# Performance work log

Hardware: AMD Instinct MI355X
Metric: run time of the kernel (lower is better)

The kernel has to match this reference:

```python
import jax, jax.numpy as jnp
import numpy as np

N, D = 12288, 128
T = 0.07  # temperature from __init__ default


def setup_inputs() -> dict:
    key = jax.random.key(0)
    x = jax.random.normal(key, (N, D), dtype=jnp.float32)
    # L2-normalize rows (this loss is defined on unit-norm embeddings;
    # keeps exp(sim / 0.07) finite in fp32 while preserving the exact math).
    x = x / jnp.linalg.norm(x, axis=-1, keepdims=True)
    return {"x": x}


def reference(x):
    # x: [N, D] -> sim: [N, N]
    sim = jnp.matmul(x, x.T) / T
    # faithful to torch: exp -> sum over last dim -> log -> mean (no LSE stabilization)
    return jnp.mean(jnp.log(jnp.sum(jnp.exp(sim), axis=-1)))
```

## Files before the change

### kernel.cpp

```cpp
#include <hip/hip_runtime.h>
#include <hip/hip_bf16.h>

#define NROWS 12288
#define DDIM  128
#define NT    96
#define CHUNK 4
#define NBLK  1200

typedef __bf16 bf16x8 __attribute__((ext_vector_type(8)));
typedef float  f32x4  __attribute__((ext_vector_type(4)));

#define GLD_LDS(g, l) __builtin_amdgcn_global_load_lds(                      \
    (const __attribute__((address_space(1))) void*)(g),                      \
    (__attribute__((address_space(3))) void*)(l), 16, 0, 0)

__device__ __forceinline__ unsigned short f2bf(float f) {
    union { float f; unsigned u; } a; a.f = f;
    unsigned r = a.u + 0x7fffu + ((a.u >> 16) & 1u);
    return (unsigned short)(r >> 16);
}

__global__ void convert_kernel(const float* __restrict__ x, unsigned short* __restrict__ xb,
                               float* __restrict__ rowsum, float* __restrict__ out) {
    int gid = blockIdx.x * 256 + threadIdx.x;
    int i = gid * 4;
    float4 v = *(const float4*)(x + i);
    ushort4 o;
    o.x = f2bf(v.x); o.y = f2bf(v.y); o.z = f2bf(v.z); o.w = f2bf(v.w);
    *(ushort4*)(xb + i) = o;
    if (gid < NROWS) rowsum[gid] = 0.f;
    if (gid == 0) out[0] = 0.f;
}

__device__ __forceinline__ void stage_tile(const unsigned short* __restrict__ xb,
                                           int row0, unsigned short* lds,
                                           int wave, int lane) {
    #pragma unroll
    for (int it = 0; it < 8; ++it) {
        int rbase = wave * 32 + it * 4;
        int r = rbase + (lane >> 4);
        int chunk = (lane & 15) ^ (r & 7);
        GLD_LDS(xb + (size_t)(row0 + r) * DDIM + chunk * 8, lds + rbase * DDIM);
    }
}

__global__ __launch_bounds__(256, 2) void gemm_exp_rowsum(
    const unsigned short* __restrict__ xb, float* __restrict__ rowsum)
{
    __shared__ __align__(16) unsigned short As[128 * DDIM];
    __shared__ __align__(16) unsigned short Bs[128 * DDIM];
    __shared__ float csumS[CHUNK * 128];
    __shared__ float rsum[128];

    const int tid = threadIdx.x;

    int rem = blockIdx.x, bi = 0;
    for (;;) {
        int nch = (NT - bi + CHUNK - 1) / CHUNK;
        if (rem < nch) break;
        rem -= nch; ++bi;
    }
    const int jt0 = bi + rem * CHUNK;
    const int ntiles = min(CHUNK, NT - jt0);
    const int i0 = bi * 128;

    for (int k = tid; k < CHUNK * 128; k += 256) csumS[k] = 0.f;
    if (tid < 128) rsum[tid] = 0.f;

    const int wave = tid >> 6, lane = tid & 63;
    const int wm = wave >> 1, wn = wave & 1;
    const int m16 = lane & 15, q = lane >> 4;

    stage_tile(xb, i0, As, wave, lane);
    stage_tile(xb, jt0 * 128, Bs, wave, lane);
    __syncthreads();

    bf16x8 af[4][4];
    #pragma unroll
    for (int mi = 0; mi < 4; ++mi) {
        int r = wm * 64 + mi * 16 + m16;
        #pragma unroll
        for (int ks = 0; ks < 4; ++ks)
            af[mi][ks] = *(const bf16x8*)(&As[r * DDIM + (((ks * 4 + q) ^ (r & 7)) * 8)]);
    }
    __syncthreads();

    const float SCALE = 20.609929155556625f;

    f32x4 rp4[4];
    #pragma unroll
    for (int mi = 0; mi < 4; ++mi) rp4[mi] = (f32x4){0.f, 0.f, 0.f, 0.f};

    unsigned short* curB = Bs;
    unsigned short* nxtB = As;

    for (int t = 0; t < ntiles; ++t) {
        const int jt = jt0 + t;

        if (t + 1 < ntiles) stage_tile(xb, (jt + 1) * 128, nxtB, wave, lane);

        f32x4 acc[4][4] = {};
        #pragma unroll
        for (int ks = 0; ks < 4; ++ks) {
            bf16x8 bfr[4];
            #pragma unroll
            for (int ni = 0; ni < 4; ++ni) {
                int r = wn * 64 + ni * 16 + m16;
                bfr[ni] = *(const bf16x8*)(&curB[r * DDIM + (((ks * 4 + q) ^ (r & 7)) * 8)]);
            }
            __builtin_amdgcn_s_setprio(1);
            #pragma unroll
            for (int mi = 0; mi < 4; ++mi)
                #pragma unroll
                for (int ni = 0; ni < 4; ++ni)
                    acc[mi][ni] = __builtin_amdgcn_mfma_f32_16x16x32_bf16(
                        af[mi][ks], bfr[ni], acc[mi][ni], 0, 0, 0);
            __builtin_amdgcn_s_setprio(0);
        }

        f32x4 cp4[4];
        #pragma unroll
        for (int ni = 0; ni < 4; ++ni) cp4[ni] = (f32x4){0.f, 0.f, 0.f, 0.f};

        #pragma unroll
        for (int mi = 0; mi < 4; ++mi)
            #pragma unroll
            for (int ni = 0; ni < 4; ++ni) {
                f32x4 sv = acc[mi][ni] * SCALE;
                f32x4 ev;
                ev[0] = __builtin_amdgcn_exp2f(sv[0]);
                ev[1] = __builtin_amdgcn_exp2f(sv[1]);
                ev[2] = __builtin_amdgcn_exp2f(sv[2]);
                ev[3] = __builtin_amdgcn_exp2f(sv[3]);
                rp4[mi] += ev;
                cp4[ni] += ev;
            }

        if (jt != bi) {
            #pragma unroll
            for (int ni = 0; ni < 4; ++ni) {
                float s = (cp4[ni][0] + cp4[ni][1]) + (cp4[ni][2] + cp4[ni][3]);
                s += __shfl_xor(s, 16);
                s += __shfl_xor(s, 32);
                if (q == 0) atomicAdd(&csumS[t * 128 + wn * 64 + ni * 16 + m16], s);
            }
        }

        __syncthreads();
        unsigned short* tmp = curB; curB = nxtB; nxtB = tmp;
    }

    #pragma unroll
    for (int mi = 0; mi < 4; ++mi)
        #pragma unroll
        for (int r = 0; r < 4; ++r) {
            float s = rp4[mi][r];
            s += __shfl_xor(s, 1);
            s += __shfl_xor(s, 2);
            s += __shfl_xor(s, 4);
            s += __shfl_xor(s, 8);
            if (m16 == 0) atomicAdd(&rsum[wm * 64 + mi * 16 + q * 4 + r], s);
        }
    __syncthreads();

    if (tid < 128) atomicAdd(&rowsum[i0 + tid], rsum[tid]);
    for (int k = tid; k < ntiles * 128; k += 256) {
        float v = csumS[k];
        if (v != 0.f) atomicAdd(&rowsum[jt0 * 128 + k], v);
    }
}

__global__ void finalize_kernel(const float* __restrict__ rowsum, float* __restrict__ out) {
    __shared__ float red[4];
    int gid = blockIdx.x * 256 + threadIdx.x;
    float lg = __logf(rowsum[gid]);
    #pragma unroll
    for (int off = 1; off < 64; off <<= 1)
        lg += __shfl_xor(lg, off);
    const int wv = threadIdx.x >> 6, ln = threadIdx.x & 63;
    if (ln == 0) red[wv] = lg;
    __syncthreads();
    if (threadIdx.x == 0)
        atomicAdd(out, (red[0] + red[1] + red[2] + red[3]) * (1.0f / (float)NROWS));
}

extern "C" void kernel_launch(void* const* d_in, const int* in_sizes, int n_in,
                              void* d_out, int out_size, void* d_ws, size_t ws_size,
                              hipStream_t stream) {
    const float* x = (const float*)d_in[0];
    float* out = (float*)d_out;

    float* rowsum = (float*)d_ws;
    unsigned short* xb = (unsigned short*)((char*)d_ws + NROWS * sizeof(float));

    convert_kernel<<<dim3((NROWS * DDIM) / (4 * 256)), dim3(256), 0, stream>>>(x, xb, rowsum, out);
    gemm_exp_rowsum<<<dim3(NBLK), dim3(256), 0, stream>>>(xb, rowsum);
    finalize_kernel<<<dim3(NROWS / 256), dim3(256), 0, stream>>>(rowsum, out);
}
```

Baseline: 105.9 us.

## Halve LDS footprint with 64-row B half-tiles and raise occupancy to four blocks

The symmetric GEMM-exp-rowsum kernel now uses a single 32 KB LDS buffer. The A tile is loaded once into registers, with each wave owning 32 rows, and the buffer is then reused as a double buffer of 64-row B half-tiles. Launch bounds go from 2 to 4 blocks per CU, and each block covers 6 column tiles instead of 4, so 816 blocks are launched instead of 1200. Row sums are atomically added straight to global memory, dropping the LDS rsum stage. The aim is more latency hiding through occupancy and fewer redundant A loads, at the cost of smaller per-wave MFMA tiles and more barriers per tile.

```diff
diff --git a/kernel.cpp b/kernel.cpp
--- a/kernel.cpp
+++ b/kernel.cpp
@@ -4,8 +4,8 @@
 #define NROWS 12288
 #define DDIM  128
 #define NT    96
-#define CHUNK 4
-#define NBLK  1200
+#define CHUNK 6
+#define NBLK  816
 
 typedef __bf16 bf16x8 __attribute__((ext_vector_type(8)));
 typedef float  f32x4  __attribute__((ext_vector_type(4)));
@@ -32,25 +32,11 @@
     if (gid == 0) out[0] = 0.f;
 }
 
-__device__ __forceinline__ void stage_tile(const unsigned short* __restrict__ xb,
-                                           int row0, unsigned short* lds,
-                                           int wave, int lane) {
-    #pragma unroll
-    for (int it = 0; it < 8; ++it) {
-        int rbase = wave * 32 + it * 4;
-        int r = rbase + (lane >> 4);
-        int chunk = (lane & 15) ^ (r & 7);
-        GLD_LDS(xb + (size_t)(row0 + r) * DDIM + chunk * 8, lds + rbase * DDIM);
-    }
-}
-
-__global__ __launch_bounds__(256, 2) void gemm_exp_rowsum(
+__global__ __launch_bounds__(256, 4) void gemm_exp_rowsum(
     const unsigned short* __restrict__ xb, float* __restrict__ rowsum)
 {
-    __shared__ __align__(16) unsigned short As[128 * DDIM];
-    __shared__ __align__(16) unsigned short Bs[128 * DDIM];
+    __shared__ __align__(16) unsigned short smem[128 * DDIM];
     __shared__ float csumS[CHUNK * 128];
-    __shared__ float rsum[128];
 
     const int tid = threadIdx.x;
 
@@ -62,55 +48,74 @@
     }
     const int jt0 = bi + rem * CHUNK;
     const int ntiles = min(CHUNK, NT - jt0);
+    const int H = 2 * ntiles;
     const int i0 = bi * 128;
 
     for (int k = tid; k < CHUNK * 128; k += 256) csumS[k] = 0.f;
-    if (tid < 128) rsum[tid] = 0.f;
 
     const int wave = tid >> 6, lane = tid & 63;
-    const int wm = wave >> 1, wn = wave & 1;
     const int m16 = lane & 15, q = lane >> 4;
 
-    stage_tile(xb, i0, As, wave, lane);
-    stage_tile(xb, jt0 * 128, Bs, wave, lane);
-    __syncthreads();
-
-    bf16x8 af[4][4];
     #pragma unroll
-    for (int mi = 0; mi < 4; ++mi) {
-        int r = wm * 64 + mi * 16 + m16;
-        #pragma unroll
-        for (int ks = 0; ks < 4; ++ks)
-            af[mi][ks] = *(const bf16x8*)(&As[r * DDIM + (((ks * 4 + q) ^ (r & 7)) * 8)]);
+    for (int it = 0; it < 8; ++it) {
+        int rbase = wave * 32 + it * 4;
+        int r = rbase + (lane >> 4);
+        int chunk = (lane & 15) ^ (r & 7);
+        GLD_LDS(xb + (size_t)(i0 + r) * DDIM + chunk * 8, smem + rbase * DDIM);
     }
     __syncthreads();
 
+    bf16x8 af[2][4];
+    #pragma unroll
+    for (int mi = 0; mi < 2; ++mi) {
+        int r = wave * 32 + mi * 16 + m16;
+        #pragma unroll
+        for (int ks = 0; ks < 4; ++ks)
+            af[mi][ks] = *(const bf16x8*)(&smem[r * DDIM + (((ks * 4 + q) ^ (r & 7)) * 8)]);
+    }
+    __syncthreads();
+
+    unsigned short* const buf0 = smem;
+    unsigned short* const buf1 = smem + 64 * DDIM;
+
+    #define STAGE_HALF(h, dst) do {                                              \
+        int jrow0_ = jt0 * 128 + (h) * 64;                                       \
+        _Pragma("unroll")                                                        \
+        for (int it = 0; it < 4; ++it) {                                         \
+            int rbase = wave * 16 + it * 4;                                      \
+            int r = rbase + (lane >> 4);                                         \
+            int chunk = (lane & 15) ^ (r & 7);                                   \
+            GLD_LDS(xb + (size_t)(jrow0_ + r) * DDIM + chunk * 8, (dst) + rbase * DDIM); \
+        }                                                                        \
+    } while (0)
+
+    STAGE_HALF(0, buf0);
+
     const float SCALE = 20.609929155556625f;
 
-    f32x4 rp4[4];
-    #pragma unroll
-    for (int mi = 0; mi < 4; ++mi) rp4[mi] = (f32x4){0.f, 0.f, 0.f, 0.f};
+    f32x4 rp4[2];
+    rp4[0] = (f32x4){0.f, 0.f, 0.f, 0.f};
+    rp4[1] = (f32x4){0.f, 0.f, 0.f, 0.f};
 
-    unsigned short* curB = Bs;
-    unsigned short* nxtB = As;
+    for (int h = 0; h < H; ++h) {
+        __syncthreads();
+        unsigned short* nxt = ((h + 1) & 1) ? buf1 : buf0;
+        if (h + 1 < H) STAGE_HALF(h + 1, nxt);
 
-    for (int t = 0; t < ntiles; ++t) {
-        const int jt = jt0 + t;
+        const unsigned short* cb = (h & 1) ? buf1 : buf0;
 
-        if (t + 1 < ntiles) stage_tile(xb, (jt + 1) * 128, nxtB, wave, lane);
-
-        f32x4 acc[4][4] = {};
+        f32x4 acc[2][4] = {};
         #pragma unroll
         for (int ks = 0; ks < 4; ++ks) {
             bf16x8 bfr[4];
             #pragma unroll
             for (int ni = 0; ni < 4; ++ni) {
-                int r = wn * 64 + ni * 16 + m16;
-                bfr[ni] = *(const bf16x8*)(&curB[r * DDIM + (((ks * 4 + q) ^ (r & 7)) * 8)]);
+                int r = ni * 16 + m16;
+                bfr[ni] = *(const bf16x8*)(&cb[r * DDIM + (((ks * 4 + q) ^ (r & 7)) * 8)]);
             }
             __builtin_amdgcn_s_setprio(1);
             #pragma unroll
-            for (int mi = 0; mi < 4; ++mi)
+            for (int mi = 0; mi < 2; ++mi)
                 #pragma unroll
                 for (int ni = 0; ni < 4; ++ni)
                     acc[mi][ni] = __builtin_amdgcn_mfma_f32_16x16x32_bf16(
@@ -118,12 +123,9 @@
             __builtin_amdgcn_s_setprio(0);
         }
 
-        f32x4 cp4[4];
+        float cp[4] = {0.f, 0.f, 0.f, 0.f};
         #pragma unroll
-        for (int ni = 0; ni < 4; ++ni) cp4[ni] = (f32x4){0.f, 0.f, 0.f, 0.f};
-
-        #pragma unroll
-        for (int mi = 0; mi < 4; ++mi)
+        for (int mi = 0; mi < 2; ++mi)
             #pragma unroll
             for (int ni = 0; ni < 4; ++ni) {
                 f32x4 sv = acc[mi][ni] * SCALE;
@@ -133,25 +135,22 @@
                 ev[2] = __builtin_amdgcn_exp2f(sv[2]);
                 ev[3] = __builtin_amdgcn_exp2f(sv[3]);
                 rp4[mi] += ev;
-                cp4[ni] += ev;
+                cp[ni] += (ev[0] + ev[1]) + (ev[2] + ev[3]);
             }
 
-        if (jt != bi) {
+        if (jt0 + (h >> 1) != bi) {
             #pragma unroll
             for (int ni = 0; ni < 4; ++ni) {
-                float s = (cp4[ni][0] + cp4[ni][1]) + (cp4[ni][2] + cp4[ni][3]);
+                float s = cp[ni];
                 s += __shfl_xor(s, 16);
                 s += __shfl_xor(s, 32);
-                if (q == 0) atomicAdd(&csumS[t * 128 + wn * 64 + ni * 16 + m16], s);
+                if (q == 0) atomicAdd(&csumS[h * 64 + ni * 16 + m16], s);
             }
         }
-
-        __syncthreads();
-        unsigned short* tmp = curB; curB = nxtB; nxtB = tmp;
     }
 
     #pragma unroll
-    for (int mi = 0; mi < 4; ++mi)
+    for (int mi = 0; mi < 2; ++mi)
         #pragma unroll
         for (int r = 0; r < 4; ++r) {
             float s = rp4[mi][r];
@@ -159,11 +158,10 @@
             s += __shfl_xor(s, 2);
             s += __shfl_xor(s, 4);
             s += __shfl_xor(s, 8);
-            if (m16 == 0) atomicAdd(&rsum[wm * 64 + mi * 16 + q * 4 + r], s);
+            if (m16 == 0) atomicAdd(&rowsum[i0 + wave * 32 + mi * 16 + q * 4 + r], s);
         }
+
     __syncthreads();
-
-    if (tid < 128) atomicAdd(&rowsum[i0 + tid], rsum[tid]);
     for (int k = tid; k < ntiles * 128; k += 256) {
         float v = csumS[k];
         if (v != 0.f) atomicAdd(&rowsum[jt0 * 128 + k], v);
```

Result: no change. 104.4 us (-1.4%).

## Pre-pack bf16 operands in MFMA fragment order and load directly from global

Applied to the files above, without the earlier changes.

The convert kernel now writes bf16 data in a fragment-major layout matching the MFMA 16x16x32 operand pattern, so each lane can load its bf16x8 fragment with one coalesced 16-byte global load. The GEMM kernel drops LDS staging, double buffering and the per-tile barrier, and instead reads B fragments straight from global/L2 into registers. The chunk size grows from 4 to 12 tiles per block (432 blocks instead of 1200), and row sums are atomically added directly to global memory instead of through a shared buffer. This removes LDS traffic and synchronization, but global load latency is now exposed with no explicit prefetch, register pressure rises, and fewer, longer blocks can balance load less evenly.

```diff
diff --git a/kernel.cpp b/kernel.cpp
--- a/kernel.cpp
+++ b/kernel.cpp
@@ -4,15 +4,11 @@
 #define NROWS 12288
 #define DDIM  128
 #define NT    96
-#define CHUNK 4
-#define NBLK  1200
+#define CHUNK 12
+#define NBLK  432
 
 typedef __bf16 bf16x8 __attribute__((ext_vector_type(8)));
 typedef float  f32x4  __attribute__((ext_vector_type(4)));
-
-#define GLD_LDS(g, l) __builtin_amdgcn_global_load_lds(                      \
-    (const __attribute__((address_space(1))) void*)(g),                      \
-    (__attribute__((address_space(3))) void*)(l), 16, 0, 0)
 
 __device__ __forceinline__ unsigned short f2bf(float f) {
     union { float f; unsigned u; } a; a.f = f;
@@ -20,37 +16,29 @@
     return (unsigned short)(r >> 16);
 }
 
-__global__ void convert_kernel(const float* __restrict__ x, unsigned short* __restrict__ xb,
+__global__ void convert_kernel(const float* __restrict__ x, unsigned short* __restrict__ xbT,
                                float* __restrict__ rowsum, float* __restrict__ out) {
     int gid = blockIdx.x * 256 + threadIdx.x;
-    int i = gid * 4;
-    float4 v = *(const float4*)(x + i);
-    ushort4 o;
-    o.x = f2bf(v.x); o.y = f2bf(v.y); o.z = f2bf(v.z); o.w = f2bf(v.w);
-    *(ushort4*)(xb + i) = o;
+    int e = gid << 3;
+    float4 v0 = *(const float4*)(x + e);
+    float4 v1 = *(const float4*)(x + e + 4);
+    uint4 o;
+    o.x = (unsigned)f2bf(v0.x) | ((unsigned)f2bf(v0.y) << 16);
+    o.y = (unsigned)f2bf(v0.z) | ((unsigned)f2bf(v0.w) << 16);
+    o.z = (unsigned)f2bf(v1.x) | ((unsigned)f2bf(v1.y) << 16);
+    o.w = (unsigned)f2bf(v1.z) | ((unsigned)f2bf(v1.w) << 16);
+    int r = gid >> 4;
+    int c = gid & 15;
+    size_t off = ((size_t)((r >> 4) * 4 + (c >> 2)) * 64 + (c & 3) * 16 + (r & 15)) * 8;
+    *(uint4*)(xbT + off) = o;
     if (gid < NROWS) rowsum[gid] = 0.f;
     if (gid == 0) out[0] = 0.f;
 }
 
-__device__ __forceinline__ void stage_tile(const unsigned short* __restrict__ xb,
-                                           int row0, unsigned short* lds,
-                                           int wave, int lane) {
-    #pragma unroll
-    for (int it = 0; it < 8; ++it) {
-        int rbase = wave * 32 + it * 4;
-        int r = rbase + (lane >> 4);
-        int chunk = (lane & 15) ^ (r & 7);
-        GLD_LDS(xb + (size_t)(row0 + r) * DDIM + chunk * 8, lds + rbase * DDIM);
-    }
-}
-
 __global__ __launch_bounds__(256, 2) void gemm_exp_rowsum(
-    const unsigned short* __restrict__ xb, float* __restrict__ rowsum)
+    const unsigned short* __restrict__ xbT, float* __restrict__ rowsum)
 {
-    __shared__ __align__(16) unsigned short As[128 * DDIM];
-    __shared__ __align__(16) unsigned short Bs[128 * DDIM];
     __shared__ float csumS[CHUNK * 128];
-    __shared__ float rsum[128];
 
     const int tid = threadIdx.x;
 
@@ -65,23 +53,18 @@
     const int i0 = bi * 128;
 
     for (int k = tid; k < CHUNK * 128; k += 256) csumS[k] = 0.f;
-    if (tid < 128) rsum[tid] = 0.f;
 
     const int wave = tid >> 6, lane = tid & 63;
-    const int wm = wave >> 1, wn = wave & 1;
     const int m16 = lane & 15, q = lane >> 4;
-
-    stage_tile(xb, i0, As, wave, lane);
-    stage_tile(xb, jt0 * 128, Bs, wave, lane);
-    __syncthreads();
+    const int wr = wave >> 1, wc = wave & 1;
 
     bf16x8 af[4][4];
     #pragma unroll
     for (int mi = 0; mi < 4; ++mi) {
-        int r = wm * 64 + mi * 16 + m16;
+        int arb = bi * 8 + wr * 4 + mi;
         #pragma unroll
         for (int ks = 0; ks < 4; ++ks)
-            af[mi][ks] = *(const bf16x8*)(&As[r * DDIM + (((ks * 4 + q) ^ (r & 7)) * 8)]);
+            af[mi][ks] = *(const bf16x8*)(xbT + ((size_t)(arb * 4 + ks) * 64 + lane) * 8);
     }
     __syncthreads();
 
@@ -91,32 +74,26 @@
     #pragma unroll
     for (int mi = 0; mi < 4; ++mi) rp4[mi] = (f32x4){0.f, 0.f, 0.f, 0.f};
 
-    unsigned short* curB = Bs;
-    unsigned short* nxtB = As;
-
     for (int t = 0; t < ntiles; ++t) {
         const int jt = jt0 + t;
 
-        if (t + 1 < ntiles) stage_tile(xb, (jt + 1) * 128, nxtB, wave, lane);
+        const unsigned short* bbase = xbT + (size_t)((jt * 8 + wc * 4) * 4) * 64 * 8;
+        bf16x8 bfr[4][4];
+        #pragma unroll
+        for (int ks = 0; ks < 4; ++ks)
+            #pragma unroll
+            for (int ni = 0; ni < 4; ++ni)
+                bfr[ks][ni] = *(const bf16x8*)(bbase + ((size_t)(ni * 4 + ks) * 64 + lane) * 8);
 
         f32x4 acc[4][4] = {};
         #pragma unroll
-        for (int ks = 0; ks < 4; ++ks) {
-            bf16x8 bfr[4];
-            #pragma unroll
-            for (int ni = 0; ni < 4; ++ni) {
-                int r = wn * 64 + ni * 16 + m16;
-                bfr[ni] = *(const bf16x8*)(&curB[r * DDIM + (((ks * 4 + q) ^ (r & 7)) * 8)]);
-            }
-            __builtin_amdgcn_s_setprio(1);
+        for (int ks = 0; ks < 4; ++ks)
             #pragma unroll
             for (int mi = 0; mi < 4; ++mi)
                 #pragma unroll
                 for (int ni = 0; ni < 4; ++ni)
                     acc[mi][ni] = __builtin_amdgcn_mfma_f32_16x16x32_bf16(
-                        af[mi][ks], bfr[ni], acc[mi][ni], 0, 0, 0);
-            __builtin_amdgcn_s_setprio(0);
-        }
+                        af[mi][ks], bfr[ks][ni], acc[mi][ni], 0, 0, 0);
 
         f32x4 cp4[4];
         #pragma unroll
@@ -142,12 +119,9 @@
                 float s = (cp4[ni][0] + cp4[ni][1]) + (cp4[ni][2] + cp4[ni][3]);
                 s += __shfl_xor(s, 16);
                 s += __shfl_xor(s, 32);
-                if (q == 0) atomicAdd(&csumS[t * 128 + wn * 64 + ni * 16 + m16], s);
+                if (q == 0) atomicAdd(&csumS[t * 128 + wc * 64 + ni * 16 + m16], s);
             }
         }
-
-        __syncthreads();
-        unsigned short* tmp = curB; curB = nxtB; nxtB = tmp;
     }
 
     #pragma unroll
@@ -159,11 +133,10 @@
             s += __shfl_xor(s, 2);
             s += __shfl_xor(s, 4);
             s += __shfl_xor(s, 8);
-            if (m16 == 0) atomicAdd(&rsum[wm * 64 + mi * 16 + q * 4 + r], s);
+            if (m16 == 0) atomicAdd(&rowsum[i0 + wr * 64 + mi * 16 + q * 4 + r], s);
         }
+
     __syncthreads();
-
-    if (tid < 128) atomicAdd(&rowsum[i0 + tid], rsum[tid]);
     for (int k = tid; k < ntiles * 128; k += 256) {
         float v = csumS[k];
         if (v != 0.f) atomicAdd(&rowsum[jt0 * 128 + k], v);
@@ -191,9 +164,9 @@
     float* out = (float*)d_out;
 
     float* rowsum = (float*)d_ws;
-    unsigned short* xb = (unsigned short*)((char*)d_ws + NROWS * sizeof(float));
+    unsigned short* xbT = (unsigned short*)((char*)d_ws + NROWS * sizeof(float));
 
-    convert_kernel<<<dim3((NROWS * DDIM) / (4 * 256)), dim3(256), 0, stream>>>(x, xb, rowsum, out);
-    gemm_exp_rowsum<<<dim3(NBLK), dim3(256), 0, stream>>>(xb, rowsum);
+    convert_kernel<<<dim3((NROWS * DDIM) / (8 * 256)), dim3(256), 0, stream>>>(x, xbT, rowsum, out);
+    gemm_exp_rowsum<<<dim3(NBLK), dim3(256), 0, stream>>>(xbT, rowsum);
     finalize_kernel<<<dim3(NROWS / 256), dim3(256), 0, stream>>>(rowsum, out);
 }
```

After: 98.22 us. 7.2% less time.
